# Kernel optimization log

Hardware: AMD Instinct MI355X
Metric: run time of the kernel (lower is better)

The kernel has to match this reference:

```python
import jax, jax.numpy as jnp
import numpy as np

NUM_EMBEDDINGS = 1024
EMBEDDING_DIM = 256


def setup_inputs() -> dict:
    key = jax.random.key(0)
    kx, kw = jax.random.split(key)
    x = jax.random.normal(kx, (64, 32, 32, EMBEDDING_DIM), dtype=jnp.float32)
    # nn.Linear(embedding_dim, num_embeddings).weight has shape [K, D]
    W = jax.random.normal(kw, (NUM_EMBEDDINGS, EMBEDDING_DIM), dtype=jnp.float32) * (1.0 / np.sqrt(EMBEDDING_DIM))
    return {"x": x, "W": W}


def reference(x, W):
    # flatten tokens: [N, D]
    flat = x.reshape(-1, EMBEDDING_DIM)
    sim = flat @ W.T
    distances = (jnp.sum(flat * flat, axis=1, keepdims=True)
                 + jnp.sum(W * W, axis=1)
                 - 2.0 * sim)
    indices = jnp.argmin(distances, axis=1)[:, None]  # [N, 1], matches torch unsqueeze(1)
    # one-hot @ W is exactly a row gather of the codebook
    quantized = jnp.take(W, indices[:, 0], axis=0).reshape(x.shape)
    return quantized, indices
```

## Files before the change

### kernel.cpp

```cpp
#include <hip/hip_runtime.h>
#include <float.h>

typedef _Float16 half8  __attribute__((ext_vector_type(8)));
typedef __fp16   fp16x2 __attribute__((ext_vector_type(2)));
typedef float    f32x16 __attribute__((ext_vector_type(16)));

#define NTOK  65536
#define DIM   256
#define NCODE 1024
#define TT    128
#define CAP   4096
#define TAU   0.08f
#define BIAS  64.0f

__device__ inline half8 pack8(float4 a, float4 b) {
    union { half8 v; fp16x2 h[4]; } u;
    u.h[0] = __builtin_amdgcn_cvt_pkrtz(a.x, a.y);
    u.h[1] = __builtin_amdgcn_cvt_pkrtz(a.z, a.w);
    u.h[2] = __builtin_amdgcn_cvt_pkrtz(b.x, b.y);
    u.h[3] = __builtin_amdgcn_cvt_pkrtz(b.z, b.w);
    return u.v;
}
__device__ inline unsigned umn(unsigned a, unsigned b) { return a < b ? a : b; }
__device__ inline unsigned umx(unsigned a, unsigned b) { return a > b ? a : b; }

__global__ __launch_bounds__(256) void prep_kernel(const float* __restrict__ W,
                                                   float* __restrict__ nw_out,
                                                   half8* __restrict__ wh_out) {
    const int k = blockIdx.x * 256 + threadIdx.x;
    const float4* wr = (const float4*)(W + (size_t)k * DIM);
    half8* dst = wh_out + (size_t)k * (DIM / 8);
    double a0 = 0.0, a1 = 0.0;
    for (int q = 0; q < DIM / 8; ++q) {
        float4 u = wr[2 * q], v = wr[2 * q + 1];
        a0 += (double)u.x * u.x + (double)u.y * u.y + (double)v.x * v.x + (double)v.y * v.y;
        a1 += (double)u.z * u.z + (double)u.w * u.w + (double)v.z * v.z + (double)v.w * v.w;
        dst[q] = pack8(u, v);
    }
    nw_out[k] = (float)(a0 + a1);
}

template <bool PRE>
__global__ __launch_bounds__(256, 2) void vq_kernel(
    const float* __restrict__ x, const float* __restrict__ W,
    const float* __restrict__ nwp, const half8* __restrict__ whp,
    float* __restrict__ outq, float* __restrict__ outidx)
{
    __shared__ _Float16 wtile[128][256];
    __shared__ float nw_s[NCODE];
    __shared__ float nx_s[TT];
    __shared__ double nxd[TT][2];
    __shared__ unsigned long long best64[TT];
    __shared__ int cnt_s;
    __shared__ int bk_s[TT];
    unsigned* cand = (unsigned*)&wtile[0][0];

    const int tid = threadIdx.x, tb = blockIdx.x * TT;
    const int wv = tid >> 6, l = tid & 63, h = l >> 5, ln = l & 31;

    if (PRE) {
        ((float4*)nw_s)[tid] = ((const float4*)nwp)[tid];
    } else {
        #pragma unroll
        for (int c = 0; c < 4; ++c) {
            const int k = (tid << 2) + c;
            const float4* wr = (const float4*)(W + (size_t)k * DIM);
            double a0 = 0.0, a1 = 0.0;
            for (int q = 0; q < DIM / 4; ++q) {
                float4 v = wr[q];
                a0 += (double)v.x * v.x + (double)v.y * v.y;
                a1 += (double)v.z * v.z + (double)v.w * v.w;
            }
            nw_s[k] = (float)(a0 + a1);
        }
    }
    {
        const int t = tid >> 1, hh = tid & 1;
        const float4* xr = (const float4*)(x + (size_t)(tb + t) * DIM + hh * 128);
        double a0 = 0.0, a1 = 0.0;
        for (int q = 0; q < 32; ++q) {
            float4 v = xr[q];
            a0 += (double)v.x * v.x + (double)v.y * v.y;
            a1 += (double)v.z * v.z + (double)v.w * v.w;
        }
        nxd[t][hh] = a0 + a1;
    }
    if (tid == 0) cnt_s = 0;
    __syncthreads();
    if (tid < TT) { nx_s[tid] = (float)(nxd[tid][0] + nxd[tid][1]); best64[tid] = ~0ull; }

    const int trow = tb + (wv << 5) + ln;
    half8 xa[16];
    #pragma unroll
    for (int s = 0; s < 16; ++s) {
        const float4* p = (const float4*)(x + (size_t)trow * DIM + (s << 4) + (h << 3));
        xa[s] = pack8(p[0], p[1]);
    }

    unsigned b0[16], b1[16];
    #pragma unroll
    for (int e = 0; e < 16; ++e) { b0[e] = 0xFFFFFFFFu; b1[e] = 0xFFFFFFFFu; }

    for (int ct = 0; ct < 8; ++ct) {
        __syncthreads();
        if (PRE) {
            half8 v[16];
            #pragma unroll
            for (int j = 0; j < 16; ++j)
                v[j] = whp[(size_t)ct * 4096 + j * 256 + tid];
            #pragma unroll
            for (int j = 0; j < 16; ++j) {
                const int g = j * 256 + tid;
                const int n = g >> 5, c = g & 31, p = c ^ (n & 31);
                *(half8*)&wtile[n][p << 3] = v[j];
            }
        } else {
            const int n = tid >> 1, hh = tid & 1;
            const float4* src = (const float4*)(W + (size_t)(ct * 128 + n) * DIM + (hh << 7));
            #pragma unroll
            for (int i = 0; i < 16; ++i) {
                float4 a = src[2 * i], b = src[2 * i + 1];
                const int c = (hh << 4) + i, p = c ^ (n & 31);
                *(half8*)&wtile[n][p << 3] = pack8(a, b);
            }
        }
        __syncthreads();

        f32x16 acc[4];
        #pragma unroll
        for (int nt = 0; nt < 4; ++nt)
            #pragma unroll
            for (int e = 0; e < 16; ++e) acc[nt][e] = 0.0f;

        #pragma unroll
        for (int sp = 0; sp < 16; ++sp) {
            const int p = ((sp << 1) + h) ^ ln;
            half8 q0 = *(const half8*)&wtile[ln     ][p << 3];
            half8 q1 = *(const half8*)&wtile[32 + ln][p << 3];
            half8 q2 = *(const half8*)&wtile[64 + ln][p << 3];
            half8 q3 = *(const half8*)&wtile[96 + ln][p << 3];
            acc[0] = __builtin_amdgcn_mfma_f32_32x32x16_f16(xa[sp], q0, acc[0], 0, 0, 0);
            acc[1] = __builtin_amdgcn_mfma_f32_32x32x16_f16(xa[sp], q1, acc[1], 0, 0, 0);
            acc[2] = __builtin_amdgcn_mfma_f32_32x32x16_f16(xa[sp], q2, acc[2], 0, 0, 0);
            acc[3] = __builtin_amdgcn_mfma_f32_32x32x16_f16(xa[sp], q3, acc[3], 0, 0, 0);
        }

        #pragma unroll
        for (int nt = 0; nt < 4; ++nt) {
            const int kk = (ct << 7) + (nt << 5) + ln;
            const float nwb = nw_s[kk] + BIAS;
            #pragma unroll
            for (int e = 0; e < 16; ++e) {
                const float c = fmaf(acc[nt][e], -2.0f, nwb);
                const unsigned u = (__float_as_uint(c) & 0xFFFFFC00u) | (unsigned)kk;
                const unsigned lo = umn(u, b0[e]), hi = umx(u, b0[e]);
                b0[e] = lo;
                b1[e] = umn(hi, b1[e]);
            }
        }
    }

    __syncthreads();

    #pragma unroll
    for (int e = 0; e < 16; ++e) {
        unsigned v = b0[e];
        #pragma unroll
        for (int m = 1; m <= 16; m <<= 1) v = umn(v, (unsigned)__shfl_xor((int)v, m));
        const float thr = __uint_as_float(v & 0xFFFFFC00u) + TAU;
        const int t = (wv << 5) + (e & 3) + ((e >> 2) << 3) + (h << 2);
        if (__uint_as_float(b0[e] & 0xFFFFFC00u) <= thr) {
            int i = atomicAdd(&cnt_s, 1);
            if (i < CAP) cand[i] = ((unsigned)t << 10) | (b0[e] & 1023u);
        }
        if (__uint_as_float(b1[e] & 0xFFFFFC00u) <= thr) {
            int i = atomicAdd(&cnt_s, 1);
            if (i < CAP) cand[i] = ((unsigned)t << 10) | (b1[e] & 1023u);
        }
    }
    __syncthreads();

    const int nc = min(cnt_s, CAP);
    for (int c = wv; c < nc; c += 4) {
        const unsigned en = cand[c];
        const int t = en >> 10, k = en & 1023;
        float4 xv = ((const float4*)(x + (size_t)(tb + t) * DIM))[l];
        float4 wr = ((const float4*)(W + (size_t)k * DIM))[l];
        float s = fmaf(xv.x, wr.x, fmaf(xv.y, wr.y, fmaf(xv.z, wr.z, xv.w * wr.w)));
        #pragma unroll
        for (int m = 1; m <= 32; m <<= 1) s += __shfl_xor(s, m);
        const float dv = (nx_s[t] + nw_s[k]) - 2.0f * s;
        if (l == 0) {
            unsigned long long key = ((unsigned long long)__float_as_uint(dv) << 32) | (unsigned)k;
            atomicMin(&best64[t], key);
        }
    }
    __syncthreads();

    if (tid < TT) {
        const int bk = (int)(best64[tid] & 1023u);
        bk_s[tid] = bk;
        outidx[tb + tid] = (float)bk;
    }
    __syncthreads();

    for (int i = tid; i < TT * (DIM / 4); i += 256) {
        const int t = i >> 6, j = i & 63;
        const float4* wr = (const float4*)(W + (size_t)bk_s[t] * DIM);
        ((float4*)(outq + (size_t)(tb + t) * DIM))[j] = wr[j];
    }
}

extern "C" void kernel_launch(void* const* d_in, const int* in_sizes, int n_in,
                              void* d_out, int out_size, void* d_ws, size_t ws_size,
                              hipStream_t stream) {
    const float* x = (const float*)d_in[0];
    const float* W = (const float*)d_in[1];
    float* outq   = (float*)d_out;
    float* outidx = outq + (size_t)NTOK * DIM;

    const size_t need = 4096 + (size_t)NCODE * DIM * sizeof(_Float16);
    if (ws_size >= need) {
        float* nw_ws = (float*)d_ws;
        half8* wh_ws = (half8*)((char*)d_ws + 4096);
        prep_kernel<<<NCODE / 256, 256, 0, stream>>>(W, nw_ws, wh_ws);
        vq_kernel<true><<<NTOK / TT, 256, 0, stream>>>(x, W, nw_ws, wh_ws, outq, outidx);
    } else {
        vq_kernel<false><<<NTOK / TT, 256, 0, stream>>>(x, W, nullptr, nullptr, outq, outidx);
    }
}
```

Measured before the change: 196.4 us.

## Halve token tile, split waves across code halves, async LDS loads

The token tile per block drops from 128 to 64. The four waves are now arranged as two token groups times two codebook halves, each wave doing a single 32x32 MFMA accumulator per 64-code tile over 16 code tiles. Occupancy is raised to 4 blocks per CU. The fp16 codebook tile is staged with global_load_lds direct-to-LDS loads, the x-norm computation is fused into the register load of x, and the prep kernel is parallelized across one row per 32 threads. These changes aim to cut register pressure and raise occupancy, at the cost of loading each x row twice and having more blocks re-read the codebook. Per-half thresholds also produce more rescoring candidates.

```diff
diff --git a/kernel.cpp b/kernel.cpp
--- a/kernel.cpp
+++ b/kernel.cpp
@@ -8,7 +8,8 @@
 #define NTOK  65536
 #define DIM   256
 #define NCODE 1024
-#define TT    128
+#define TT    64
+#define NCT   16
 #define CAP   4096
 #define TAU   0.08f
 #define BIAS  64.0f
@@ -24,32 +25,38 @@
 __device__ inline unsigned umn(unsigned a, unsigned b) { return a < b ? a : b; }
 __device__ inline unsigned umx(unsigned a, unsigned b) { return a > b ? a : b; }
 
+__device__ inline void gload16(const void* g, void* l) {
+    __builtin_amdgcn_global_load_lds(
+        (__attribute__((address_space(1))) void*)(size_t)g,
+        (__attribute__((address_space(3))) void*)l,
+        16, 0, 0);
+}
+
 __global__ __launch_bounds__(256) void prep_kernel(const float* __restrict__ W,
                                                    float* __restrict__ nw_out,
                                                    half8* __restrict__ wh_out) {
-    const int k = blockIdx.x * 256 + threadIdx.x;
-    const float4* wr = (const float4*)(W + (size_t)k * DIM);
-    half8* dst = wh_out + (size_t)k * (DIM / 8);
-    double a0 = 0.0, a1 = 0.0;
-    for (int q = 0; q < DIM / 8; ++q) {
-        float4 u = wr[2 * q], v = wr[2 * q + 1];
-        a0 += (double)u.x * u.x + (double)u.y * u.y + (double)v.x * v.x + (double)v.y * v.y;
-        a1 += (double)u.z * u.z + (double)u.w * u.w + (double)v.z * v.z + (double)v.w * v.w;
-        dst[q] = pack8(u, v);
-    }
-    nw_out[k] = (float)(a0 + a1);
+    const int tid = threadIdx.x;
+    const int k = blockIdx.x * 8 + (tid >> 5);
+    const int c = tid & 31;
+    const float4* wr = (const float4*)(W + (size_t)k * DIM + c * 8);
+    float4 u = wr[0], v = wr[1];
+    wh_out[(size_t)k * 32 + c] = pack8(u, v);
+    double a = (double)u.x * u.x + (double)u.y * u.y + (double)u.z * u.z + (double)u.w * u.w
+             + (double)v.x * v.x + (double)v.y * v.y + (double)v.z * v.z + (double)v.w * v.w;
+    #pragma unroll
+    for (int m = 1; m <= 16; m <<= 1) a += __shfl_xor(a, m);
+    if (c == 0) nw_out[k] = (float)a;
 }
 
 template <bool PRE>
-__global__ __launch_bounds__(256, 2) void vq_kernel(
+__global__ __launch_bounds__(256, 4) void vq_kernel(
     const float* __restrict__ x, const float* __restrict__ W,
     const float* __restrict__ nwp, const half8* __restrict__ whp,
     float* __restrict__ outq, float* __restrict__ outidx)
 {
-    __shared__ _Float16 wtile[128][256];
+    __shared__ _Float16 wtile[64][256];
     __shared__ float nw_s[NCODE];
     __shared__ float nx_s[TT];
-    __shared__ double nxd[TT][2];
     __shared__ unsigned long long best64[TT];
     __shared__ int cnt_s;
     __shared__ int bk_s[TT];
@@ -57,6 +64,8 @@
 
     const int tid = threadIdx.x, tb = blockIdx.x * TT;
     const int wv = tid >> 6, l = tid & 63, h = l >> 5, ln = l & 31;
+    const int tg = wv & 1;
+    const int ch = wv >> 1;
 
     if (PRE) {
         ((float4*)nw_s)[tid] = ((const float4*)nwp)[tid];
@@ -74,89 +83,73 @@
             nw_s[k] = (float)(a0 + a1);
         }
     }
-    {
-        const int t = tid >> 1, hh = tid & 1;
-        const float4* xr = (const float4*)(x + (size_t)(tb + t) * DIM + hh * 128);
-        double a0 = 0.0, a1 = 0.0;
-        for (int q = 0; q < 32; ++q) {
-            float4 v = xr[q];
-            a0 += (double)v.x * v.x + (double)v.y * v.y;
-            a1 += (double)v.z * v.z + (double)v.w * v.w;
-        }
-        nxd[t][hh] = a0 + a1;
-    }
     if (tid == 0) cnt_s = 0;
-    __syncthreads();
-    if (tid < TT) { nx_s[tid] = (float)(nxd[tid][0] + nxd[tid][1]); best64[tid] = ~0ull; }
-
-    const int trow = tb + (wv << 5) + ln;
+    if (tid < TT) best64[tid] = ~0ull;
+
+    const int trow = tb + (tg << 5) + ln;
     half8 xa[16];
+    double a0 = 0.0, a1 = 0.0;
     #pragma unroll
     for (int s = 0; s < 16; ++s) {
         const float4* p = (const float4*)(x + (size_t)trow * DIM + (s << 4) + (h << 3));
-        xa[s] = pack8(p[0], p[1]);
+        float4 u = p[0], v = p[1];
+        xa[s] = pack8(u, v);
+        if (ch == 0) {
+            a0 += (double)u.x * u.x + (double)u.y * u.y + (double)v.x * v.x + (double)v.y * v.y;
+            a1 += (double)u.z * u.z + (double)u.w * u.w + (double)v.z * v.z + (double)v.w * v.w;
+        }
+    }
+    if (ch == 0) {
+        double nx = a0 + a1;
+        nx += __shfl_xor(nx, 32);
+        if (h == 0) nx_s[(tg << 5) + ln] = (float)nx;
     }
 
     unsigned b0[16], b1[16];
     #pragma unroll
     for (int e = 0; e < 16; ++e) { b0[e] = 0xFFFFFFFFu; b1[e] = 0xFFFFFFFFu; }
 
-    for (int ct = 0; ct < 8; ++ct) {
+    for (int ct = 0; ct < NCT; ++ct) {
         __syncthreads();
         if (PRE) {
-            half8 v[16];
             #pragma unroll
-            for (int j = 0; j < 16; ++j)
-                v[j] = whp[(size_t)ct * 4096 + j * 256 + tid];
-            #pragma unroll
-            for (int j = 0; j < 16; ++j) {
+            for (int j = 0; j < 8; ++j) {
                 const int g = j * 256 + tid;
-                const int n = g >> 5, c = g & 31, p = c ^ (n & 31);
-                *(half8*)&wtile[n][p << 3] = v[j];
+                const int src = (g & ~31) | ((g & 31) ^ ((g >> 5) & 31));
+                gload16(whp + (size_t)ct * 2048 + src, (_Float16*)&wtile[0][0] + (size_t)g * 8);
             }
         } else {
-            const int n = tid >> 1, hh = tid & 1;
-            const float4* src = (const float4*)(W + (size_t)(ct * 128 + n) * DIM + (hh << 7));
+            const int n = tid >> 2, qq = tid & 3;
+            const float4* srcp = (const float4*)(W + (size_t)(ct * 64 + n) * DIM + (qq << 6));
             #pragma unroll
-            for (int i = 0; i < 16; ++i) {
-                float4 a = src[2 * i], b = src[2 * i + 1];
-                const int c = (hh << 4) + i, p = c ^ (n & 31);
+            for (int i = 0; i < 8; ++i) {
+                float4 a = srcp[2 * i], b = srcp[2 * i + 1];
+                const int c = (qq << 3) + i, p = c ^ (n & 31);
                 *(half8*)&wtile[n][p << 3] = pack8(a, b);
             }
         }
         __syncthreads();
 
-        f32x16 acc[4];
-        #pragma unroll
-        for (int nt = 0; nt < 4; ++nt)
-            #pragma unroll
-            for (int e = 0; e < 16; ++e) acc[nt][e] = 0.0f;
+        f32x16 acc;
+        #pragma unroll
+        for (int e = 0; e < 16; ++e) acc[e] = 0.0f;
 
         #pragma unroll
         for (int sp = 0; sp < 16; ++sp) {
             const int p = ((sp << 1) + h) ^ ln;
-            half8 q0 = *(const half8*)&wtile[ln     ][p << 3];
-            half8 q1 = *(const half8*)&wtile[32 + ln][p << 3];
-            half8 q2 = *(const half8*)&wtile[64 + ln][p << 3];
-            half8 q3 = *(const half8*)&wtile[96 + ln][p << 3];
-            acc[0] = __builtin_amdgcn_mfma_f32_32x32x16_f16(xa[sp], q0, acc[0], 0, 0, 0);
-            acc[1] = __builtin_amdgcn_mfma_f32_32x32x16_f16(xa[sp], q1, acc[1], 0, 0, 0);
-            acc[2] = __builtin_amdgcn_mfma_f32_32x32x16_f16(xa[sp], q2, acc[2], 0, 0, 0);
-            acc[3] = __builtin_amdgcn_mfma_f32_32x32x16_f16(xa[sp], q3, acc[3], 0, 0, 0);
-        }
-
-        #pragma unroll
-        for (int nt = 0; nt < 4; ++nt) {
-            const int kk = (ct << 7) + (nt << 5) + ln;
-            const float nwb = nw_s[kk] + BIAS;
-            #pragma unroll
-            for (int e = 0; e < 16; ++e) {
-                const float c = fmaf(acc[nt][e], -2.0f, nwb);
-                const unsigned u = (__float_as_uint(c) & 0xFFFFFC00u) | (unsigned)kk;
-                const unsigned lo = umn(u, b0[e]), hi = umx(u, b0[e]);
-                b0[e] = lo;
-                b1[e] = umn(hi, b1[e]);
-            }
+            half8 q = *(const half8*)&wtile[(ch << 5) + ln][p << 3];
+            acc = __builtin_amdgcn_mfma_f32_32x32x16_f16(xa[sp], q, acc, 0, 0, 0);
+        }
+
+        const int kk = (ct << 6) + (ch << 5) + ln;
+        const float nwb = nw_s[kk] + BIAS;
+        #pragma unroll
+        for (int e = 0; e < 16; ++e) {
+            const float c = fmaf(acc[e], -2.0f, nwb);
+            const unsigned u = (__float_as_uint(c) & 0xFFFFFC00u) | (unsigned)kk;
+            const unsigned lo = umn(u, b0[e]), hi = umx(u, b0[e]);
+            b0[e] = lo;
+            b1[e] = umn(hi, b1[e]);
         }
     }
 
@@ -168,7 +161,7 @@
         #pragma unroll
         for (int m = 1; m <= 16; m <<= 1) v = umn(v, (unsigned)__shfl_xor((int)v, m));
         const float thr = __uint_as_float(v & 0xFFFFFC00u) + TAU;
-        const int t = (wv << 5) + (e & 3) + ((e >> 2) << 3) + (h << 2);
+        const int t = (tg << 5) + (e & 3) + ((e >> 2) << 3) + (h << 2);
         if (__uint_as_float(b0[e] & 0xFFFFFC00u) <= thr) {
             int i = atomicAdd(&cnt_s, 1);
             if (i < CAP) cand[i] = ((unsigned)t << 10) | (b0[e] & 1023u);
@@ -223,7 +216,7 @@
     if (ws_size >= need) {
         float* nw_ws = (float*)d_ws;
         half8* wh_ws = (half8*)((char*)d_ws + 4096);
-        prep_kernel<<<NCODE / 256, 256, 0, stream>>>(W, nw_ws, wh_ws);
+        prep_kernel<<<NCODE / 8, 256, 0, stream>>>(W, nw_ws, wh_ws);
         vq_kernel<true><<<NTOK / TT, 256, 0, stream>>>(x, W, nw_ws, wh_ws, outq, outidx);
     } else {
         vq_kernel<false><<<NTOK / TT, 256, 0, stream>>>(x, W, nullptr, nullptr, outq, outidx);
```

After: 267.8 us. +36.4%, slower.
